# Kernel optimization log

Hardware: AMD Instinct MI355X
Metric: run time of the kernel (lower is better)

Reference implementation:

```python
import jax, jax.numpy as jnp
import numpy as np

NUM_HEADS = 16
DIM = 1024

def setup_inputs() -> dict:
    key = jax.random.key(0)
    ks = jax.random.split(key, 12)
    B, N, T, C = 4, 4096, 77, DIM
    s = 1.0 / np.sqrt(C)
    return {
        "hidden_states": jax.random.normal(ks[0], (B, N, C), jnp.float32),
        "encoder_hidden_states": jax.random.normal(ks[1], (B, T, C), jnp.float32),
        "attention_mask": jnp.zeros((B, N, T), jnp.float32),
        "Wq": jax.random.normal(ks[2], (C, C), jnp.float32) * s,
        "bq": jnp.zeros((C,), jnp.float32),
        "Wk": jax.random.normal(ks[3], (C, C), jnp.float32) * s,
        "bk": jnp.zeros((C,), jnp.float32),
        "Wv": jax.random.normal(ks[4], (C, C), jnp.float32) * s,
        "bv": jnp.zeros((C,), jnp.float32),
        "Wo": jax.random.normal(ks[5], (C, C), jnp.float32) * s,
        "bo": jnp.zeros((C,), jnp.float32),
    }

def reference(hidden_states, encoder_hidden_states, attention_mask,
              Wq, bq, Wk, bk, Wv, bv, Wo, bo):
    B, N, C = hidden_states.shape
    T = encoder_hidden_states.shape[1]
    H = NUM_HEADS
    D = C // H
    # QKV projections (torch Linear: x @ W.T + b)
    q = (hidden_states @ Wq.T + bq).reshape(B, N, H, D).transpose(0, 2, 1, 3)   # bhnd
    k = (encoder_hidden_states @ Wk.T + bk).reshape(B, T, H, D).transpose(0, 2, 1, 3)  # bhtd
    v = (encoder_hidden_states @ Wv.T + bv).reshape(B, T, H, D).transpose(0, 2, 1, 3)  # bhtd
    scale = 1.0 / jnp.sqrt(jnp.asarray(D, q.dtype))
    # scores [B,H,N,T]; additive mask broadcast over heads
    scores = jnp.einsum('bhnd,bhtd->bhnt', q, k) * scale + attention_mask[:, None, :, :]
    attn = jax.nn.softmax(scores, axis=-1)
    out = jnp.einsum('bhnt,bhtd->bhnd', attn, v)
    out = out.transpose(0, 2, 1, 3).reshape(B, N, C)
    return out @ Wo.T + bo
```

## Files before the change

kernel.cpp:

```cpp
#include <hip/hip_runtime.h>
#include <cstdint>

typedef __bf16 bf16x8 __attribute__((ext_vector_type(8)));
typedef float f32x4 __attribute__((ext_vector_type(4)));
typedef unsigned short u16;
typedef unsigned int u32;

__device__ __forceinline__ u16 f2bf(float f) {
    u32 u = __builtin_bit_cast(u32, f);
    u += 0x7fffu + ((u >> 16) & 1u);
    return (u16)(u >> 16);
}

__device__ __forceinline__ void gl_lds16(const u16* g, u16* l) {
    __builtin_amdgcn_global_load_lds(
        (const __attribute__((address_space(1))) void*)g,
        (__attribute__((address_space(3))) void*)l,
        16, 0, 0);
}

__device__ __forceinline__ f32x4 mfma16(bf16x8 a, bf16x8 b, f32x4 c) {
    return __builtin_amdgcn_mfma_f32_16x16x32_bf16(a, b, c, 0, 0, 0);
}


struct CvtAll {
    const float* s[6];
    u16* d[6];
    int srcn[6];
    int totn[6];
    int off[6];
};

__global__ void cvt_all(CvtAll a) {
    const int blk = blockIdx.x;
    int seg = 0;
#pragma unroll
    for (int s = 1; s < 6; ++s) seg += (blk >= a.off[s]);
    const int i = ((blk - a.off[seg]) * 256 + threadIdx.x) * 4;
    if (i >= a.totn[seg]) return;
    float4 v = make_float4(0.f, 0.f, 0.f, 0.f);
    if (i < a.srcn[seg]) v = *(const float4*)&a.s[seg][i];
    ushort4 o;
    o.x = f2bf(v.x); o.y = f2bf(v.y); o.z = f2bf(v.z); o.w = f2bf(v.w);
    *(ushort4*)&a.d[seg][i] = o;
}

__device__ __forceinline__ void store_out(u16* C, long idx, float v) { C[idx] = f2bf(v); }
__device__ __forceinline__ void store_out(float* C, long idx, float v) { C[idx] = v; }

template <typename OutT, bool BA, bool BC>
__global__ __launch_bounds__(512, 2) void gemmP(
    const u16* __restrict__ A, const u16* __restrict__ W,
    const float* __restrict__ bias, OutT* __restrict__ C,
    int M, int N, int K) {
    __shared__ __align__(16) u16 As[3][256 * 32];
    __shared__ __align__(16) u16 Bs[3][128 * 32];

    const int tid = threadIdx.x;
    const int wid = tid >> 6, l = tid & 63;
    const int wr = wid >> 1, wc = wid & 1;
    const int l15 = l & 15, lg = l >> 4;

    const int lin = blockIdx.y * gridDim.x + blockIdx.x;
    const int cpx = (gridDim.x * gridDim.y) >> 3;
    const int swz = (lin & 7) * cpx + (lin >> 3);
    const long tn = swz & 7;
    const long tm = swz >> 3;

    const int srp = tid >> 3;
    const int sv = (tid & 7) ^ (srp & 7);
    const int sE = (sv >> 2) & 1;
    const int sKC = sv & 3;
    const long ar0 = tm * 256 + 2 * srp + sE;
    const long brow = tn * 128 + 2 * srp + sE;
    const long aRB = ar0 >> 2;
    const int aSub = (int)(ar0 & 3) * 16 + (sKC & 1) * 8;
    const int aCB = sKC >> 1;

    const int NT = K >> 5;

#define STAGE(s_, t_)                                                          \
    do {                                                                       \
        if (BA) {                                                              \
            const long cb_ = (long)((t_) * 2 + aCB) * (M >> 2);                \
            gl_lds16(A + (cb_ + aRB) * 64 + aSub, &As[s_][tid * 8]);           \
            gl_lds16(A + (cb_ + aRB + 32) * 64 + aSub,                         \
                     &As[s_][4096 + tid * 8]);                                 \
        } else {                                                               \
            gl_lds16(A + ar0 * (long)K + (t_) * 32 + sKC * 8,                  \
                     &As[s_][tid * 8]);                                        \
            gl_lds16(A + (ar0 + 128) * (long)K + (t_) * 32 + sKC * 8,          \
                     &As[s_][4096 + tid * 8]);                                 \
        }                                                                      \
        gl_lds16(W + brow * (long)K + (t_) * 32 + sKC * 8,                     \
                 &Bs[s_][tid * 8]);                                            \
    } while (0)

    const int e = l15 & 1;
    const int rphA = wr * 32 + (l15 >> 1);
    const int rphB = wc * 32 + (l15 >> 1);
    const int pA = ((e * 4 + lg) ^ (rphA & 7)) * 8;
    const int pB = ((e * 4 + lg) ^ (rphB & 7)) * 8;
    const int aOff = rphA * 64 + pA;
    const int bOff = rphB * 64 + pB;

    f32x4 acc[4][4] = {};

    STAGE(0, 0);
    STAGE(1, 1);

    for (int t = 0; t < NT; ++t) {
        if (t + 1 < NT)
            asm volatile("s_waitcnt vmcnt(3)" ::: "memory");
        else
            asm volatile("s_waitcnt vmcnt(0)" ::: "memory");
        __builtin_amdgcn_sched_barrier(0);
        __builtin_amdgcn_s_barrier();

        if (t + 2 < NT) {
            const int ns = (t + 2) % 3;
            STAGE(ns, t + 2);
        }

        const int c = t % 3;
        bf16x8 a[4], b[4];
#pragma unroll
        for (int nf = 0; nf < 4; ++nf)
            b[nf] = *(const bf16x8*)&Bs[c][bOff + nf * 512];
#pragma unroll
        for (int mf = 0; mf < 4; ++mf)
            a[mf] = *(const bf16x8*)&As[c][aOff + mf * 512];

        __builtin_amdgcn_s_setprio(1);
#pragma unroll
        for (int mf = 0; mf < 4; ++mf)
#pragma unroll
            for (int nf = 0; nf < 4; ++nf)
                acc[mf][nf] = mfma16(a[mf], b[nf], acc[mf][nf]);
        __builtin_amdgcn_s_setprio(0);
    }
#undef STAGE

    const long row0 = tm * 256 + wr * 64;
    const long col0 = tn * 128 + wc * 64;
    float bv[4];
#pragma unroll
    for (int nf = 0; nf < 4; ++nf) bv[nf] = bias[col0 + nf * 16 + l15];
    if (BC) {
        const long ct0 = col0 >> 4;
        const long rb = row0 >> 2;
#pragma unroll
        for (int mf = 0; mf < 4; ++mf)
#pragma unroll
            for (int nf = 0; nf < 4; ++nf)
#pragma unroll
                for (int r = 0; r < 4; ++r) {
                    const long idx =
                        ((ct0 + nf) * (long)(M >> 2) + rb + mf * 4 + lg) * 64 +
                        r * 16 + l15;
                    store_out(C, idx, acc[mf][nf][r] + bv[nf]);
                }
    } else {
#pragma unroll
        for (int mf = 0; mf < 4; ++mf)
#pragma unroll
            for (int nf = 0; nf < 4; ++nf)
#pragma unroll
                for (int r = 0; r < 4; ++r) {
                    const long row = row0 + mf * 16 + lg * 4 + r;
                    const long col = col0 + nf * 16 + l15;
                    store_out(C, row * N + col, acc[mf][nf][r] + bv[nf]);
                }
    }
}

template <bool VT>
__device__ __forceinline__ void gemm128_body(
    const u16* __restrict__ A, const u16* __restrict__ W,
    const float* __restrict__ bias, u16* __restrict__ C,
    int N, int K) {
    __shared__ u16 As[128 * 64];
    __shared__ u16 Bs[128 * 64];
    const int tid = threadIdx.x;
    const int w = tid >> 6, l = tid & 63;
    const int wr = w >> 1, wc = w & 1;
    const int l15 = l & 15, lg = l >> 4;
    const long tm = blockIdx.y, tn = blockIdx.x;
    const u16* Ab = A + tm * 128 * (long)K;
    const u16* Bb = W + tn * 128 * (long)K;

    f32x4 acc[4][4] = {};

    for (int k0 = 0; k0 < K; k0 += 64) {
#pragma unroll
        for (int t = 0; t < 4; ++t) {
            int i = t * 256 + tid;
            int row = i >> 3, cc = i & 7;
            gl_lds16(Ab + (long)row * K + k0 + cc * 8, &As[i * 8]);
            gl_lds16(Bb + (long)row * K + k0 + cc * 8, &Bs[i * 8]);
        }
        __syncthreads();
#pragma unroll
        for (int kk = 0; kk < 64; kk += 32) {
            bf16x8 a[4], b[4];
#pragma unroll
            for (int m = 0; m < 4; ++m)
                a[m] = *(const bf16x8*)&As[(wr * 64 + m * 16 + l15) * 64 + kk + lg * 8];
#pragma unroll
            for (int n = 0; n < 4; ++n)
                b[n] = *(const bf16x8*)&Bs[(wc * 64 + n * 16 + l15) * 64 + kk + lg * 8];
#pragma unroll
            for (int m = 0; m < 4; ++m)
#pragma unroll
                for (int n = 0; n < 4; ++n)
                    acc[m][n] = mfma16(a[m], b[n], acc[m][n]);
        }
        __syncthreads();
    }

    const long row0 = tm * 128 + wr * 64;
    const long col0 = tn * 128 + wc * 64;
#pragma unroll
    for (int m = 0; m < 4; ++m)
#pragma unroll
        for (int n = 0; n < 4; ++n)
#pragma unroll
            for (int r = 0; r < 4; ++r) {
                const float v = acc[m][n][r] + bias[col0 + n * 16 + l15];
                if (VT) {
                    const int row = (int)(row0 + m * 16 + lg * 4 + r);
                    if (row < 308) {
                        const int bb = row / 77;
                        const int t = row - bb * 77;
                        const int ch = (int)(col0 + n * 16 + l15);
                        const long idx = (long)bb * 98304 +
                                         ((long)(t >> 4) * 256 + (ch >> 2)) * 64 +
                                         (ch & 3) * 16 + (t & 15);
                        C[idx] = f2bf(v);
                    }
                } else {
                    const long idx = (((col0 >> 4) + n) * 96L + (row0 >> 2) + m * 4 + lg) * 64 +
                                     r * 16 + l15;
                    C[idx] = f2bf(v);
                }
            }
}

__global__ __launch_bounds__(256) void gemm_kv(
    const u16* __restrict__ A,
    const u16* __restrict__ Wk, const float* __restrict__ bk, u16* __restrict__ Ko,
    const u16* __restrict__ Wv, const float* __restrict__ bv, u16* __restrict__ Vo,
    int N, int K) {
    if (blockIdx.z == 0)
        gemm128_body<false>(A, Wk, bk, Ko, N, K);
    else
        gemm128_body<true>(A, Wv, bv, Vo, N, K);
}

__global__ __launch_bounds__(256, 4) void attn_fused(
    const u16* __restrict__ Q,
    const u16* __restrict__ Kb,
    const u16* __restrict__ Vt,
    const float* __restrict__ mask,
    u16* __restrict__ Ao) {
    __shared__ u16 Ps[128 * 104];

    const int h = blockIdx.x, b = blockIdx.y, nt = blockIdx.z;
    const int tid = threadIdx.x;
    const int w = tid >> 6, l = tid & 63;
    const int l15 = l & 15, lg = l >> 4;

    const int qrow = b * 4096 + nt * 128 + w * 32;

    f32x4 acc[5][2] = {};
#pragma unroll
    for (int kk = 0; kk < 64; kk += 32) {
        const int d = kk + lg * 8;
        const int cb = h * 4 + (d >> 4);
        const int dlow = d & 15;
        bf16x8 kf[5], qf[2];
#pragma unroll
        for (int n = 0; n < 5; ++n) {
            const int row = b * 77 + n * 16 + l15;
            kf[n] = *(const bf16x8*)&Kb[((long)cb * 96 + (row >> 2)) * 64 +
                                        (row & 3) * 16 + dlow];
        }
#pragma unroll
        for (int m = 0; m < 2; ++m) {
            const int row = qrow + m * 16 + l15;
            qf[m] = *(const bf16x8*)&Q[((long)cb * 4096 + (row >> 2)) * 64 +
                                       (row & 3) * 16 + dlow];
        }
#pragma unroll
        for (int n = 0; n < 5; ++n)
#pragma unroll
            for (int m = 0; m < 2; ++m)
                acc[n][m] = mfma16(kf[n], qf[m], acc[n][m]);
    }

    const float* mrow0 = mask + ((long)b * 4096 + nt * 128 + w * 32) * 77;
#pragma unroll
    for (int m = 0; m < 2; ++m) {
        const float* mrow = mrow0 + (m * 16 + l15) * 77;
        float vals[5][4];
        float rmax = -3e38f;
#pragma unroll
        for (int n = 0; n < 5; ++n) {
            const int t0 = n * 16 + lg * 4;
#pragma unroll
            for (int r = 0; r < 4; ++r) {
                float mv;
                if (n < 4)
                    mv = mrow[t0 + r];
                else
                    mv = (t0 + r < 77) ? mrow[t0 + r] : -1e30f;
                const float v = acc[n][m][r] * 0.125f + mv;
                vals[n][r] = v;
                rmax = fmaxf(rmax, v);
            }
        }
        rmax = fmaxf(rmax, __shfl_xor(rmax, 16, 64));
        rmax = fmaxf(rmax, __shfl_xor(rmax, 32, 64));
        float s = 0.f;
#pragma unroll
        for (int n = 0; n < 5; ++n)
#pragma unroll
            for (int r = 0; r < 4; ++r) {
                const float e = __expf(vals[n][r] - rmax);
                vals[n][r] = e;
                s += e;
            }
        s += __shfl_xor(s, 16, 64);
        s += __shfl_xor(s, 32, 64);
        const float inv = 1.f / s;
#pragma unroll
        for (int n = 0; n < 5; ++n) {
            const u32 lo = (u32)f2bf(vals[n][0] * inv) |
                           ((u32)f2bf(vals[n][1] * inv) << 16);
            const u32 hi = (u32)f2bf(vals[n][2] * inv) |
                           ((u32)f2bf(vals[n][3] * inv) << 16);
            *(uint2*)&Ps[(w * 32 + m * 16 + l15) * 104 + n * 16 + lg * 4] =
                make_uint2(lo, hi);
        }
        *(uint2*)&Ps[(w * 32 + m * 16 + l15) * 104 + 80 + lg * 4] = make_uint2(0, 0);
    }

    f32x4 o[2][4] = {};
#pragma unroll
    for (int kt = 0; kt < 96; kt += 32) {
        bf16x8 pa[2], vf[4];
#pragma unroll
        for (int m = 0; m < 2; ++m)
            pa[m] = *(const bf16x8*)&Ps[(w * 32 + m * 16 + l15) * 104 + kt + lg * 8];
        const int t0 = kt + lg * 8;
#pragma unroll
        for (int n = 0; n < 4; ++n) {
            const int ch = h * 64 + n * 16 + l15;
            vf[n] = *(const bf16x8*)&Vt[(long)b * 98304 +
                                        ((long)(t0 >> 4) * 256 + (ch >> 2)) * 64 +
                                        (ch & 3) * 16 + (t0 & 15)];
        }
#pragma unroll
        for (int m = 0; m < 2; ++m)
#pragma unroll
            for (int n = 0; n < 4; ++n)
                o[m][n] = mfma16(pa[m], vf[n], o[m][n]);
    }

#pragma unroll
    for (int m = 0; m < 2; ++m)
#pragma unroll
        for (int n = 0; n < 4; ++n)
#pragma unroll
            for (int r = 0; r < 4; ++r) {
                const long idx = ((long)(h * 4 + n) * 4096 +
                                  b * 1024 + nt * 32 + w * 8 + m * 4 + lg) * 64 +
                                 r * 16 + l15;
                Ao[idx] = f2bf(o[m][n][r]);
            }
}

extern "C" void kernel_launch(void* const* d_in, const int* in_sizes, int n_in,
                              void* d_out, int out_size, void* d_ws, size_t ws_size,
                              hipStream_t stream) {
    const float* hidden = (const float*)d_in[0];
    const float* enc = (const float*)d_in[1];
    const float* mask = (const float*)d_in[2];
    const float* Wq = (const float*)d_in[3];
    const float* bq = (const float*)d_in[4];
    const float* Wk = (const float*)d_in[5];
    const float* bk = (const float*)d_in[6];
    const float* Wv = (const float*)d_in[7];
    const float* bv = (const float*)d_in[8];
    const float* Wo = (const float*)d_in[9];
    const float* bo = (const float*)d_in[10];
    float* out = (float*)d_out;

    char* ws = (char*)d_ws;
    u16* hiddenB = (u16*)(ws);
    u16* Qb = (u16*)(ws + 33554432L);
    u16* AoB = (u16*)(ws + 2 * 33554432L);
    u16* WqB = (u16*)(ws + 3 * 33554432L);
    u16* WkB = WqB + 1048576;
    u16* WvB = WkB + 1048576;
    u16* WoB = WvB + 1048576;
    u16* encB = WoB + 1048576;
    u16* Kbuf = encB + 393216;
    u16* VtBuf = Kbuf + 393216;

    CvtAll ca;
    ca.s[0] = hidden; ca.d[0] = hiddenB; ca.srcn[0] = 16777216; ca.totn[0] = 16777216;
    ca.s[1] = Wq;  ca.d[1] = WqB; ca.srcn[1] = 1048576; ca.totn[1] = 1048576;
    ca.s[2] = Wk;  ca.d[2] = WkB; ca.srcn[2] = 1048576; ca.totn[2] = 1048576;
    ca.s[3] = Wv;  ca.d[3] = WvB; ca.srcn[3] = 1048576; ca.totn[3] = 1048576;
    ca.s[4] = Wo;  ca.d[4] = WoB; ca.srcn[4] = 1048576; ca.totn[4] = 1048576;
    ca.s[5] = enc; ca.d[5] = encB; ca.srcn[5] = 315392; ca.totn[5] = 393216;
    ca.off[0] = 0;
    ca.off[1] = 16384;
    ca.off[2] = 17408;
    ca.off[3] = 18432;
    ca.off[4] = 19456;
    ca.off[5] = 20480;
    cvt_all<<<dim3(20864), 256, 0, stream>>>(ca);

    gemmP<u16, false, true><<<dim3(8, 64), 512, 0, stream>>>(
        hiddenB, WqB, bq, Qb, 16384, 1024, 1024);
    gemm_kv<<<dim3(8, 3, 2), 256, 0, stream>>>(encB, WkB, bk, Kbuf, WvB, bv, VtBuf, 1024, 1024);

    attn_fused<<<dim3(16, 4, 32), 256, 0, stream>>>(Qb, Kbuf, VtBuf, mask, AoB);

    gemmP<float, true, false><<<dim3(8, 64), 512, 0, stream>>>(
        AoB, WoB, bo, out, 16384, 1024, 1024);
}
```

Before: 161.4 us.

## Double-buffer and swizzle KV GEMM LDS; stage attention mask through LDS as bf16

The KV projection GEMM now uses two LDS buffers, so the next K tile is prefetched while the current one is multiplied, and one barrier per iteration is dropped. An XOR swizzle on the LDS column index is meant to avoid bank conflicts on the fragment reads. In the attention kernel the mask tile is loaded with coalesced reads into LDS as bf16 instead of strided per-lane global reads. Occupancy is lowered to 3 blocks per CU to fit the extra LDS. Mask precision drops to bf16, which only matters for nonzero masks.

```diff
diff --git a/kernel.cpp b/kernel.cpp
--- a/kernel.cpp
+++ b/kernel.cpp
@@ -10,6 +10,10 @@
     u32 u = __builtin_bit_cast(u32, f);
     u += 0x7fffu + ((u >> 16) & 1u);
     return (u16)(u >> 16);
+}
+
+__device__ __forceinline__ float bf2f(u32 x) {
+    return __builtin_bit_cast(float, x << 16);
 }
 
 __device__ __forceinline__ void gl_lds16(const u16* g, u16* l) {
@@ -180,8 +184,8 @@
     const u16* __restrict__ A, const u16* __restrict__ W,
     const float* __restrict__ bias, u16* __restrict__ C,
     int N, int K) {
-    __shared__ u16 As[128 * 64];
-    __shared__ u16 Bs[128 * 64];
+    __shared__ __align__(16) u16 As[2][128 * 64];
+    __shared__ __align__(16) u16 Bs[2][128 * 64];
     const int tid = threadIdx.x;
     const int w = tid >> 6, l = tid & 63;
     const int wr = w >> 1, wc = w & 1;
@@ -190,34 +194,54 @@
     const u16* Ab = A + tm * 128 * (long)K;
     const u16* Bb = W + tn * 128 * (long)K;
 
+    const int srow = tid >> 3;
+    const int skc = (tid & 7) ^ (srow & 7);
+
+#define KV_STAGE(s_, k0_)                                                     \
+    do {                                                                      \
+        _Pragma("unroll")                                                     \
+        for (int j_ = 0; j_ < 4; ++j_) {                                      \
+            gl_lds16(Ab + (long)(srow + j_ * 32) * K + (k0_) + skc * 8,       \
+                     &As[s_][j_ * 2048 + tid * 8]);                           \
+            gl_lds16(Bb + (long)(srow + j_ * 32) * K + (k0_) + skc * 8,       \
+                     &Bs[s_][j_ * 2048 + tid * 8]);                           \
+        }                                                                     \
+    } while (0)
+
     f32x4 acc[4][4] = {};
-
-    for (int k0 = 0; k0 < K; k0 += 64) {
-#pragma unroll
-        for (int t = 0; t < 4; ++t) {
-            int i = t * 256 + tid;
-            int row = i >> 3, cc = i & 7;
-            gl_lds16(Ab + (long)row * K + k0 + cc * 8, &As[i * 8]);
-            gl_lds16(Bb + (long)row * K + k0 + cc * 8, &Bs[i * 8]);
+    const int NT = K >> 6;
+
+    KV_STAGE(0, 0);
+    __syncthreads();
+
+    for (int t = 0; t < NT; ++t) {
+        const int c = t & 1;
+        if (t + 1 < NT) KV_STAGE(c ^ 1, (t + 1) << 6);
+
+#pragma unroll
+        for (int kk = 0; kk < 2; ++kk) {
+            bf16x8 a[4], bb[4];
+#pragma unroll
+            for (int m = 0; m < 4; ++m) {
+                const int ar = wr * 64 + m * 16 + l15;
+                const int cc = (kk * 4 + lg) ^ (ar & 7);
+                a[m] = *(const bf16x8*)&As[c][ar * 64 + cc * 8];
+            }
+#pragma unroll
+            for (int n = 0; n < 4; ++n) {
+                const int br = wc * 64 + n * 16 + l15;
+                const int cc = (kk * 4 + lg) ^ (br & 7);
+                bb[n] = *(const bf16x8*)&Bs[c][br * 64 + cc * 8];
+            }
+#pragma unroll
+            for (int m = 0; m < 4; ++m)
+#pragma unroll
+                for (int n = 0; n < 4; ++n)
+                    acc[m][n] = mfma16(a[m], bb[n], acc[m][n]);
         }
         __syncthreads();
-#pragma unroll
-        for (int kk = 0; kk < 64; kk += 32) {
-            bf16x8 a[4], b[4];
-#pragma unroll
-            for (int m = 0; m < 4; ++m)
-                a[m] = *(const bf16x8*)&As[(wr * 64 + m * 16 + l15) * 64 + kk + lg * 8];
-#pragma unroll
-            for (int n = 0; n < 4; ++n)
-                b[n] = *(const bf16x8*)&Bs[(wc * 64 + n * 16 + l15) * 64 + kk + lg * 8];
-#pragma unroll
-            for (int m = 0; m < 4; ++m)
-#pragma unroll
-                for (int n = 0; n < 4; ++n)
-                    acc[m][n] = mfma16(a[m], b[n], acc[m][n]);
-        }
-        __syncthreads();
-    }
+    }
+#undef KV_STAGE
 
     const long row0 = tm * 128 + wr * 64;
     const long col0 = tn * 128 + wc * 64;
@@ -258,18 +282,37 @@
         gemm128_body<true>(A, Wv, bv, Vo, N, K);
 }
 
-__global__ __launch_bounds__(256, 4) void attn_fused(
+__global__ __launch_bounds__(256, 3) void attn_fused(
     const u16* __restrict__ Q,
     const u16* __restrict__ Kb,
     const u16* __restrict__ Vt,
     const float* __restrict__ mask,
     u16* __restrict__ Ao) {
     __shared__ u16 Ps[128 * 104];
+    __shared__ u16 Ms[128 * 88];
 
     const int h = blockIdx.x, b = blockIdx.y, nt = blockIdx.z;
     const int tid = threadIdx.x;
     const int w = tid >> 6, l = tid & 63;
     const int l15 = l & 15, lg = l >> 4;
+
+    {
+        const float* mb = mask + ((long)b * 4096 + nt * 128) * 77;
+        const int lane = tid & 63;
+        const int rg = tid >> 6;
+#pragma unroll
+        for (int g = 0; g < 32; ++g) {
+            const int row = g * 4 + rg;
+            const long rb = (long)row * 77;
+            Ms[row * 88 + lane] = f2bf(mb[rb + lane]);
+            const int t2 = lane + 64;
+            if (t2 < 80) {
+                const float v1 = (t2 < 77) ? mb[rb + t2] : -1e38f;
+                Ms[row * 88 + t2] = f2bf(v1);
+            }
+        }
+    }
+    __syncthreads();
 
     const int qrow = b * 4096 + nt * 128 + w * 32;
 
@@ -299,26 +342,24 @@
                 acc[n][m] = mfma16(kf[n], qf[m], acc[n][m]);
     }
 
-    const float* mrow0 = mask + ((long)b * 4096 + nt * 128 + w * 32) * 77;
 #pragma unroll
     for (int m = 0; m < 2; ++m) {
-        const float* mrow = mrow0 + (m * 16 + l15) * 77;
+        const int lrow = w * 32 + m * 16 + l15;
         float vals[5][4];
         float rmax = -3e38f;
 #pragma unroll
         for (int n = 0; n < 5; ++n) {
-            const int t0 = n * 16 + lg * 4;
-#pragma unroll
-            for (int r = 0; r < 4; ++r) {
-                float mv;
-                if (n < 4)
-                    mv = mrow[t0 + r];
-                else
-                    mv = (t0 + r < 77) ? mrow[t0 + r] : -1e30f;
-                const float v = acc[n][m][r] * 0.125f + mv;
-                vals[n][r] = v;
-                rmax = fmaxf(rmax, v);
-            }
+            const uint2 mm = *(const uint2*)&Ms[lrow * 88 + n * 16 + lg * 4];
+            const float mv0 = bf2f(mm.x & 0xffffu);
+            const float mv1 = bf2f(mm.x >> 16);
+            const float mv2 = bf2f(mm.y & 0xffffu);
+            const float mv3 = bf2f(mm.y >> 16);
+            vals[n][0] = fmaf(acc[n][m][0], 0.125f, mv0);
+            vals[n][1] = fmaf(acc[n][m][1], 0.125f, mv1);
+            vals[n][2] = fmaf(acc[n][m][2], 0.125f, mv2);
+            vals[n][3] = fmaf(acc[n][m][3], 0.125f, mv3);
+#pragma unroll
+            for (int r = 0; r < 4; ++r) rmax = fmaxf(rmax, vals[n][r]);
         }
         rmax = fmaxf(rmax, __shfl_xor(rmax, 16, 64));
         rmax = fmaxf(rmax, __shfl_xor(rmax, 32, 64));
```

After: 199.6 us. +23.7%, slower.
